# Optimization experiments

Hardware: AMD Instinct MI355X
Metric: run time of the kernel (lower is better)

Reference implementation:

```python
import jax, jax.numpy as jnp
import numpy as np

B, L_ENC, L_DEC, PRED_LEN = 16, 720, 144, 96
D_MODEL, N_HEADS, D_FF, M_FEAT = 512, 8, 2048, 256
ENC_IN, DEC_IN, C_OUT, MARK = 7, 7, 7, 4
E_LAYERS = 2
DH = D_MODEL // N_HEADS


def _orf(m, d, seed):
    # Gaussian orthogonal random features (FAVOR+), scaling=0 (chi-norm rows).
    rng = np.random.default_rng(seed)
    blocks = [np.linalg.qr(rng.standard_normal((d, d)))[0].T for _ in range(m // d)]
    mat = np.concatenate(blocks, 0)  # [m, d]
    mult = np.linalg.norm(rng.standard_normal((m, d)), axis=1)
    return jnp.asarray(mult[:, None] * mat, dtype=jnp.float32)

PROJ_ENC = [_orf(M_FEAT, DH, s) for s in range(E_LAYERS)]
PROJ_DEC_SELF = _orf(M_FEAT, DH, 10)
PROJ_DEC_CROSS = _orf(M_FEAT, DH, 11)


def _pos_emb(n, d):
    pos = np.arange(n, dtype=np.float32)[:, None]
    div = np.exp(np.arange(0, d, 2, dtype=np.float32) * (-np.log(10000.0) / d))
    pe = np.zeros((n, d), dtype=np.float32)
    pe[:, 0::2] = np.sin(pos * div)
    pe[:, 1::2] = np.cos(pos * div)
    return jnp.asarray(pe)

PE_ENC = _pos_emb(L_ENC, D_MODEL)
PE_DEC = _pos_emb(L_DEC, D_MODEL)


def layer_norm(x, g, b):
    mu = x.mean(-1, keepdims=True)
    var = ((x - mu) ** 2).mean(-1, keepdims=True)
    return (x - mu) / jnp.sqrt(var + 1e-5) * g + b


def feature_map(x, proj, is_query):
    # FAVOR+ positive softmax kernel. x: [b,h,n,dh], proj: [m,dh]
    norm = DH ** -0.25
    xd = jnp.einsum('bhnd,md->bhnm', x * norm, proj)
    diag = (x ** 2).sum(-1) * (0.5 * norm * norm)  # [b,h,n]
    if is_query:
        stab = jax.lax.stop_gradient(xd.max(axis=-1, keepdims=True))
    else:
        stab = jax.lax.stop_gradient(xd.max(axis=(-1, -2), keepdims=True))
    return (M_FEAT ** -0.5) * (jnp.exp(xd - diag[..., None] - stab) + 1e-4)


def noncausal_attn(q, k, v):
    kv = jnp.einsum('bhnm,bhnd->bhmd', k, v)
    d_inv = 1.0 / jnp.einsum('bhnm,bhm->bhn', q, k.sum(2))
    return jnp.einsum('bhnm,bhmd,bhn->bhnd', q, kv, d_inv)


def causal_attn(q, k, v):
    # prefix-sum linear attention; carry S [b,h,m,dh], s [b,h,m]
    b, h, n, m = q.shape
    dh = v.shape[-1]

    def step(carry, qkv):
        S, s = carry
        qn, kn, vn = qkv
        S = S + kn[..., None] * vn[..., None, :]
        s = s + kn
        num = jnp.einsum('bhm,bhmd->bhd', qn, S)
        den = jnp.einsum('bhm,bhm->bh', qn, s)
        return (S, s), num / (den[..., None] + 1e-6)

    init = (jnp.zeros((b, h, m, dh), q.dtype), jnp.zeros((b, h, m), q.dtype))
    _, out = jax.lax.scan(step, init, (jnp.moveaxis(q, 2, 0), jnp.moveaxis(k, 2, 0), jnp.moveaxis(v, 2, 0)))
    return jnp.moveaxis(out, 0, 2)


def attention(x, ctx, Wq, Wk, Wv, Wo, bo, proj, causal):
    b, n, _ = x.shape
    nc = ctx.shape[1]
    q = (x @ Wq).reshape(b, n, N_HEADS, DH).transpose(0, 2, 1, 3)
    k = (ctx @ Wk).reshape(b, nc, N_HEADS, DH).transpose(0, 2, 1, 3)
    v = (ctx @ Wv).reshape(b, nc, N_HEADS, DH).transpose(0, 2, 1, 3)
    qp = feature_map(q, proj, True)
    kp = feature_map(k, proj, False)
    o = causal_attn(qp, kp, v) if causal else noncausal_attn(qp, kp, v)
    o = o.transpose(0, 2, 1, 3).reshape(b, n, D_MODEL)
    return o @ Wo + bo


def embed(x, mark, conv_w, time_w, pe):
    # TokenEmbedding: circular conv1d k=3 (no bias) + fixed sinusoidal PE + timeF linear
    xp = jnp.concatenate([x[:, -1:], x, x[:, :1]], axis=1)
    tok = (jnp.einsum('blc,cd->bld', xp[:, :-2], conv_w[0])
           + jnp.einsum('blc,cd->bld', xp[:, 1:-1], conv_w[1])
           + jnp.einsum('blc,cd->bld', xp[:, 2:], conv_w[2]))
    return tok + pe[None] + mark @ time_w


def _forward(x_enc, x_mark_enc, x_dec, x_mark_dec,
             emb_conv_enc, emb_time_enc, emb_conv_dec, emb_time_dec,
             enc_Wq, enc_Wk, enc_Wv, enc_Wo, enc_bo,
             enc_ff1, enc_b1, enc_ff2, enc_b2, enc_ln_g, enc_ln_b, enc_fg, enc_fb,
             dec_sWq, dec_sWk, dec_sWv, dec_sWo, dec_sbo,
             dec_cWq, dec_cWk, dec_cWv, dec_cWo, dec_cbo,
             dec_ff1, dec_b1, dec_ff2, dec_b2, dec_ln_g, dec_ln_b, dec_fg, dec_fb,
             proj_w, proj_b):
    gelu = lambda t: jax.nn.gelu(t, approximate=False)
    # RevIN-style instance normalization (means detached, as in the torch code)
    means = jax.lax.stop_gradient(x_enc.mean(1, keepdims=True))
    xc = x_enc - means
    stdev = jnp.sqrt(xc.var(1, keepdims=True) + 1e-5)
    xe = xc / stdev

    enc = embed(xe, x_mark_enc, emb_conv_enc, emb_time_enc, PE_ENC)
    for i in range(E_LAYERS):
        a = attention(enc, enc, enc_Wq[i], enc_Wk[i], enc_Wv[i], enc_Wo[i], enc_bo[i], PROJ_ENC[i], False)
        x1 = layer_norm(enc + a, enc_ln_g[i, 0], enc_ln_b[i, 0])
        y = gelu(x1 @ enc_ff1[i] + enc_b1[i]) @ enc_ff2[i] + enc_b2[i]
        enc = layer_norm(x1 + y, enc_ln_g[i, 1], enc_ln_b[i, 1])
    enc = layer_norm(enc, enc_fg, enc_fb)

    dec = embed(x_dec, x_mark_dec, emb_conv_dec, emb_time_dec, PE_DEC)
    a = attention(dec, dec, dec_sWq, dec_sWk, dec_sWv, dec_sWo, dec_sbo, PROJ_DEC_SELF, True)
    x1 = layer_norm(dec + a, dec_ln_g[0], dec_ln_b[0])
    c = attention(x1, enc, dec_cWq, dec_cWk, dec_cWv, dec_cWo, dec_cbo, PROJ_DEC_CROSS, False)
    x2 = layer_norm(x1 + c, dec_ln_g[1], dec_ln_b[1])
    y = gelu(x2 @ dec_ff1 + dec_b1) @ dec_ff2 + dec_b2
    dec = layer_norm(x2 + y, dec_ln_g[2], dec_ln_b[2])
    dec = layer_norm(dec, dec_fg, dec_fb)
    out = dec @ proj_w + proj_b  # [B, L_DEC, C_OUT]

    out = out * stdev[:, 0][:, None, :] + means[:, 0][:, None, :]
    return out[:, -PRED_LEN:, :]


def setup_inputs():
    ks = iter(jax.random.split(jax.random.key(0), 48))

    def rn(shape, scale=1.0):
        return jax.random.normal(next(ks), shape, dtype=jnp.float32) * scale

    w = 0.02
    E, D, F = E_LAYERS, D_MODEL, D_FF
    return {
        'x_enc': rn((B, L_ENC, ENC_IN)),
        'x_mark_enc': rn((B, L_ENC, MARK)),
        'x_dec': rn((B, L_DEC, DEC_IN)),
        'x_mark_dec': rn((B, L_DEC, MARK)),
        'emb_conv_enc': rn((3, ENC_IN, D), 0.1),
        'emb_time_enc': rn((MARK, D), w),
        'emb_conv_dec': rn((3, DEC_IN, D), 0.1),
        'emb_time_dec': rn((MARK, D), w),
        'enc_Wq': rn((E, D, D), w), 'enc_Wk': rn((E, D, D), w),
        'enc_Wv': rn((E, D, D), w), 'enc_Wo': rn((E, D, D), w),
        'enc_bo': jnp.zeros((E, D), jnp.float32),
        'enc_ff1': rn((E, D, F), w), 'enc_b1': jnp.zeros((E, F), jnp.float32),
        'enc_ff2': rn((E, F, D), w), 'enc_b2': jnp.zeros((E, D), jnp.float32),
        'enc_ln_g': jnp.ones((E, 2, D), jnp.float32), 'enc_ln_b': jnp.zeros((E, 2, D), jnp.float32),
        'enc_fg': jnp.ones((D,), jnp.float32), 'enc_fb': jnp.zeros((D,), jnp.float32),
        'dec_sWq': rn((D, D), w), 'dec_sWk': rn((D, D), w), 'dec_sWv': rn((D, D), w), 'dec_sWo': rn((D, D), w),
        'dec_sbo': jnp.zeros((D,), jnp.float32),
        'dec_cWq': rn((D, D), w), 'dec_cWk': rn((D, D), w), 'dec_cWv': rn((D, D), w), 'dec_cWo': rn((D, D), w),
        'dec_cbo': jnp.zeros((D,), jnp.float32),
        'dec_ff1': rn((D, F), w), 'dec_b1': jnp.zeros((F,), jnp.float32),
        'dec_ff2': rn((F, D), w), 'dec_b2': jnp.zeros((D,), jnp.float32),
        'dec_ln_g': jnp.ones((3, D), jnp.float32), 'dec_ln_b': jnp.zeros((3, D), jnp.float32),
        'dec_fg': jnp.ones((D,), jnp.float32), 'dec_fb': jnp.zeros((D,), jnp.float32),
        'proj_w': rn((D, C_OUT), w), 'proj_b': jnp.zeros((C_OUT,), jnp.float32),
    }


def reference(x_enc, x_mark_enc, x_dec, x_mark_dec,
              emb_conv_enc, emb_time_enc, emb_conv_dec, emb_time_dec,
              enc_Wq, enc_Wk, enc_Wv, enc_Wo, enc_bo,
              enc_ff1, enc_b1, enc_ff2, enc_b2, enc_ln_g, enc_ln_b, enc_fg, enc_fb,
              dec_sWq, dec_sWk, dec_sWv, dec_sWo, dec_sbo,
              dec_cWq, dec_cWk, dec_cWv, dec_cWo, dec_cbo,
              dec_ff1, dec_b1, dec_ff2, dec_b2, dec_ln_g, dec_ln_b, dec_fg, dec_fb,
              proj_w, proj_b):
    return _forward(x_enc, x_mark_enc, x_dec, x_mark_dec,
                    emb_conv_enc, emb_time_enc, emb_conv_dec, emb_time_dec,
                    enc_Wq, enc_Wk, enc_Wv, enc_Wo, enc_bo,
                    enc_ff1, enc_b1, enc_ff2, enc_b2, enc_ln_g, enc_ln_b, enc_fg, enc_fb,
                    dec_sWq, dec_sWk, dec_sWv, dec_sWo, dec_sbo,
                    dec_cWq, dec_cWk, dec_cWv, dec_cWo, dec_cbo,
                    dec_ff1, dec_b1, dec_ff2, dec_b2, dec_ln_g, dec_ln_b, dec_fg, dec_fb,
                    proj_w, proj_b)
```

## Files before the change

### kernel.cpp

```cpp
#include <hip/hip_runtime.h>
#include <math.h>
#include <string.h>

#define BB    16
#define LEc   720
#define LDc   144
#define PREDc 96
#define DMc   512
#define NHc   8
#define DHc   64
#define MFc   256
#define FFc   2048
#define NEc   (BB*LEc)
#define NDc   (BB*LDc)
#define BHc   (BB*NHc)
#define KSn   ((size_t)BHc*MFc)

typedef unsigned int u32;
typedef unsigned short u16;
typedef unsigned long long u64;
typedef unsigned __int128 u128;

typedef short bfx8 __attribute__((ext_vector_type(8)));
typedef float fx4  __attribute__((ext_vector_type(4)));
// ... 105 lines not shown
    if (xnorm == 0.0){
      tau[j] = 0.0;
      for (int i=j;i<n;i++) V[j][i] = (i==j) ? 1.0 : 0.0;
      continue;
    }
    double beta = -copysign(hypot(alpha, xnorm), alpha);
    double tj = (beta - alpha)/beta;
    double sc = 1.0/(alpha - beta);
    tau[j] = tj;
    V[j][j] = 1.0;
    for (int i=j+1;i<n;i++) V[j][i] = A[i*n+j]*sc;
    A[j*n+j] = beta;
    for (int c=j+1;c<n;c++){
      double w = 0;
      for (int i=j;i<n;i++) w += V[j][i]*A[i*n+c];
      w *= tj;
      for (int i=j;i<n;i++) A[i*n+c] -= V[j][i]*w;
    }
  }
  for (int i=0;i<n;i++) for (int c=0;c<n;c++) Q[i*n+c] = (i==c)?1.0:0.0;
  for (int j=n-1;j>=0;j--){
    double tj = tau[j];
    if (tj == 0.0) continue;
    for (int c=0;c<n;c++){
      double w = 0;
      for (int i=j;i<n;i++) w += V[j][i]*Q[i*n+c];
      w *= tj;
      for (int i=j;i<n;i++) Q[i*n+c] -= V[j][i]*w;
    }
  }
}

static void build_orf(u32 seed, float* outp){
  NpPCG64 g(seed);
  static double mat[MFc][DHc];
  static double A[64*64], Q[64*64];
  for (int blk=0; blk<4; blk++){
    for (int i=0;i<4096;i++) A[i] = std_normal(g);
    qr_q64(A, Q);
    for (int r=0;r<64;r++)
      for (int c=0;c<64;c++)
        mat[blk*64 + r][c] = Q[c*64 + r];
  }
  for (int r=0;r<MFc;r++){
    double ss = 0;
    double row[64];
    for (int c=0;c<64;c++){ row[c] = std_normal(g); ss += row[c]*row[c]; }
    double nrm = sqrt(ss);
    for (int c=0;c<64;c++) outp[r*64 + c] = (float)(nrm * mat[r][c]);
  }
}

static void build_all_proj(float* h){
  init_zig();
  const u32 seeds[4] = {0u, 1u, 10u, 11u};
  for (int s=0;s<4;s++) build_orf(seeds[s], h + (size_t)s*MFc*DHc);
}

__device__ __forceinline__ u16 f2bf(float x){
  u32 u = __builtin_bit_cast(u32, x);
  u32 r = (u + 0x7FFFu + ((u >> 16) & 1u)) >> 16;
  return (u16)r;
}
__device__ __forceinline__ float bf2f(u16 x){
  return __builtin_bit_cast(float, ((u32)x) << 16);
}


__global__ __launch_bounds__(256) void k_zero(float* __restrict__ p, int n){
  int i = blockIdx.x*256 + threadIdx.x;
  if (i < n) p[i] = 0.f;
}

__global__ __launch_bounds__(256) void k_projbf(const float* __restrict__ p, u16* __restrict__ pb, int n){
  int i = blockIdx.x*256 + threadIdx.x;
  if (i < n) pb[i] = f2bf(p[i]);
}

__global__ __launch_bounds__(256) void k_petab(float* __restrict__ pe){
  int idx = blockIdx.x*256 + threadIdx.x;
  int d = idx & 511; int l = idx >> 9;
  int i2 = d & ~1;
  float div = expf((float)i2 * (-0.017988946039015984f));
  float ang = (float)l * div;
  pe[idx] = (d & 1) ? cosf(ang) : sinf(ang);
}

__global__ __launch_bounds__(256) void k_wtr(const float* __restrict__ W, u16* __restrict__ WT,
                                             int K, int N){
  __shared__ float t[32][33];
  int kb = blockIdx.x*32, nb = blockIdx.y*32;
  int tx = threadIdx.x & 31, ty = threadIdx.x >> 5;
  #pragma unroll
  for (int p=0;p<4;p++)
    t[ty + p*8][tx] = W[(size_t)(kb + ty + p*8)*N + nb + tx];
  __syncthreads();
  #pragma unroll
  for (int p=0;p<4;p++)
    WT[(size_t)(nb + ty + p*8)*K + kb + tx] = f2bf(t[tx][ty + p*8]);
}

__global__ __launch_bounds__(64) void k_meanstd(const float* __restrict__ x,
                                                float* __restrict__ means, float* __restrict__ stdev){
  int bc = blockIdx.x; int b = bc/7, c = bc%7;
  int t = threadIdx.x;
  float s=0;
  for (int l=t; l<LEc; l+=64) s += x[((size_t)b*LEc+l)*7 + c];
  for (int o=32;o;o>>=1) s += __shfl_down(s,o);
  s = __shfl(s,0);
  float mu = s / (float)LEc;
  float v=0;
  for (int l=t; l<LEc; l+=64){ float d = x[((size_t)b*LEc+l)*7+c]-mu; v += d*d; }
  for (int o=32;o;o>>=1) v += __shfl_down(v,o);
  if (t==0){ means[bc]=mu; stdev[bc]=sqrtf(v/(float)LEc + 1e-5f); }
}

__global__ __launch_bounds__(256) void k_embed(const float* __restrict__ x, const float* __restrict__ mark,
    const float* __restrict__ convw, const float* __restrict__ timew, const float* __restrict__ pe,
    const float* __restrict__ means, const float* __restrict__ stdev,
    int L, int donorm, float* __restrict__ outp)
{
  size_t idx = (size_t)blockIdx.x*256 + threadIdx.x;
  size_t total = (size_t)BB*L*DMc;
  if (idx >= total) return;
  int d = (int)(idx % DMc); size_t bl = idx / DMc; int l = (int)(bl % L); int b = (int)(bl / L);
  int lm = (l==0)? L-1 : l-1;
  int lp = (l==L-1)? 0 : l+1;
  float acc = pe[(size_t)l*DMc + d];
  const float* xb = x + (size_t)b*L*7;
  #pragma unroll
  for (int c=0;c<7;c++){
    float v0 = xb[(size_t)lm*7+c], v1 = xb[(size_t)l*7+c], v2 = xb[(size_t)lp*7+c];
    if (donorm){
      float mu = means[b*7+c], sd = stdev[b*7+c];
      v0=(v0-mu)/sd; v1=(v1-mu)/sd; v2=(v2-mu)/sd;
    }
    acc += v0*convw[(0*7+c)*DMc+d] + v1*convw[(1*7+c)*DMc+d] + v2*convw[(2*7+c)*DMc+d];
  }
  const float* mb = mark + ((size_t)b*L + l)*4;
  #pragma unroll
  for (int t=0;t<4;t++) acc += mb[t]*timew[t*DMc+d];
  outp[idx] = acc;
}

template<int A_BF16, int OUT_BF16, int GELU>
__global__ __launch_bounds__(256) void k_gemm_mfma(
    const void* __restrict__ Ap, const u16* __restrict__ WT,
    const float* __restrict__ bias, void* __restrict__ Cp,
    int M, int N, int K)
{
  __shared__ u16 As[128][40];
  __shared__ u16 Bs[128][40];
  int nb = N >> 7;
  int bx = blockIdx.x % nb, by = blockIdx.x / nb;
  int row0 = by << 7, col0 = bx << 7;
  int tid = threadIdx.x;
  int wid = tid >> 6, lane = tid & 63;
  int wr = (wid >> 1) * 64, wc = (wid & 1) * 64;
  int l15 = lane & 15, lg = lane >> 4;
  fx4 acc[4][4];
  #pragma unroll
  for (int i=0;i<4;i++)
    #pragma unroll
    for (int j=0;j<4;j++)
      #pragma unroll
      for (int r=0;r<4;r++) acc[i][j][r] = 0.f;

  for (int k0 = 0; k0 < K; k0 += 32){
    if (A_BF16){
      const u16* A = (const u16*)Ap;
      #pragma unroll
      for (int p=0;p<2;p++){
        int idx = tid + (p<<8);
        int r = idx >> 2, kq = (idx & 3) << 3;
        *(bfx8*)&As[r][kq] = *(const bfx8*)(A + (size_t)(row0+r)*K + k0 + kq);
      }
    } else {
      const float* A = (const float*)Ap;
      #pragma unroll
      for (int p=0;p<4;p++){
        int idx = tid + (p<<8);
        int r = idx >> 3, kq = (idx & 7) << 2;
        float4 v = *(const float4*)(A + (size_t)(row0+r)*K + k0 + kq);
        u32 lo = (u32)f2bf(v.x) | ((u32)f2bf(v.y) << 16);
        u32 hi = (u32)f2bf(v.z) | ((u32)f2bf(v.w) << 16);
        *(u32*)&As[r][kq]   = lo;
        *(u32*)&As[r][kq+2] = hi;
      }
    }
    #pragma unroll
    for (int p=0;p<2;p++){
      int idx = tid + (p<<8);
      int c = idx >> 2, kq = (idx & 3) << 3;
      *(bfx8*)&Bs[c][kq] = *(const bfx8*)(WT + (size_t)(col0+c)*K + k0 + kq);
    }
    __syncthreads();
    int kg = lg << 3;
    bfx8 af[4], bf[4];
    #pragma unroll
    for (int i=0;i<4;i++) af[i] = *(const bfx8*)&As[wr + i*16 + l15][kg];
    #pragma unroll
    for (int j=0;j<4;j++) bf[j] = *(const bfx8*)&Bs[wc + j*16 + l15][kg];
    #pragma unroll
    for (int i=0;i<4;i++)
      #pragma unroll
      for (int j=0;j<4;j++)
        acc[i][j] = __builtin_amdgcn_mfma_f32_16x16x32_bf16(af[i], bf[j], acc[i][j], 0, 0, 0);
    __syncthreads();
  }
  #pragma unroll
  for (int j=0;j<4;j++){
    int col = col0 + wc + j*16 + l15;
    float bv = bias ? bias[col] : 0.f;
    #pragma unroll
    for (int i=0;i<4;i++){
      #pragma unroll
      for (int r=0;r<4;r++){
        int row = row0 + wr + i*16 + (lg<<2) + r;
        float v = acc[i][j][r] + bv;
        if (GELU) v = 0.5f*v*(1.0f + erff(v*0.7071067811865475f));
        if (OUT_BF16) ((u16*)Cp)[(size_t)row*N + col] = f2bf(v);
        else          ((float*)Cp)[(size_t)row*N + col] = v;
      }
    }
  }
}

static inline void gemm_bf(const void* A, const u16* WT, const float* bias, void* C,
                           int M, int N, int K, int abf, int obf, int gelu, hipStream_t st){
  dim3 g((N/128)*(M/128));
  if (abf)            k_gemm_mfma<1,0,0><<<g,256,0,st>>>(A,WT,bias,C,M,N,K);
  else if (gelu)      k_gemm_mfma<0,1,1><<<g,256,0,st>>>(A,WT,bias,C,M,N,K);
  else if (obf)       k_gemm_mfma<0,1,0><<<g,256,0,st>>>(A,WT,bias,C,M,N,K);
  else                k_gemm_mfma<0,0,0><<<g,256,0,st>>>(A,WT,bias,C,M,N,K);
}

__global__ __launch_bounds__(256) void k_rowmax_mfma(const u16* __restrict__ Kb,
    const u16* __restrict__ projbf, float* __restrict__ rowmax, int n)
{
  int ntile = n >> 4;
  int rt = blockIdx.x % ntile, bh = blockIdx.x / ntile;
  int b = bh >> 3, h = bh & 7;
  int row0 = rt << 4;
  int tid = threadIdx.x, w = tid >> 6, lane = tid & 63;
  int l15 = lane & 15, lg = lane >> 4;
  __shared__ u16 qs[16][72];
  __shared__ float xds[16][264];
  __shared__ float red[16][16];
  for (int i = tid; i < 16*16; i += 256){
    int r = i >> 4, dq = (i & 15)*4;
    *(u16x4*)&qs[r][dq] = *(const u16x4*)(Kb + ((size_t)b*n + row0 + r)*DMc + h*64 + dq);
  }
  __syncthreads();
  #pragma unroll
  for (int mt=0; mt<4; mt++){
    int m16 = (w*4+mt)*16;
    fx4 a2 = {0.f,0.f,0.f,0.f};
    #pragma unroll
    for (int ks=0; ks<2; ks++){
      bfx8 af = *(const bfx8*)&qs[l15][ks*32 + lg*8];
      bfx8 bf = *(const bfx8*)(projbf + (size_t)(m16+l15)*64 + ks*32 + lg*8);
      a2 = __builtin_amdgcn_mfma_f32_16x16x32_bf16(af, bf, a2, 0, 0, 0);
    }
    #pragma unroll
    for (int r=0;r<4;r++)
      xds[lg*4+r][m16+l15] = a2[r];
  }
  __syncthreads();
  { int r = tid >> 4, s = tid & 15;
    float mx = -1e30f;
    #pragma unroll
    for (int j=0;j<16;j++) mx = fmaxf(mx, xds[r][s*16+j]);
    red[r][s] = mx; }
  __syncthreads();
  if (tid < 16){
    float mx = -1e30f;
    #pragma unroll
    for (int j=0;j<16;j++) mx = fmaxf(mx, red[tid][j]);
    rowmax[(size_t)bh*n + row0 + tid] = mx * 0.35355339059327373f;
  }
}

__global__ __launch_bounds__(256) void k_stab(const float* __restrict__ rowmax, float* __restrict__ stab, int n){
  int bh = blockIdx.x; int tid = threadIdx.x;
  float mx = -1e30f;
  for (int i=tid;i<n;i+=256) mx = fmaxf(mx, rowmax[(size_t)bh*n+i]);
  __shared__ float red[4];
  for (int o=32;o;o>>=1) mx = fmaxf(mx, __shfl_xor(mx,o));
  if ((tid&63)==0) red[tid>>6]=mx;
  __syncthreads();
  if (tid==0) stab[bh] = fmaxf(fmaxf(red[0],red[1]),fmaxf(red[2],red[3]));
}

__global__ __launch_bounds__(256) void k_vtr(const u16* __restrict__ Vb, u16* __restrict__ Vt, int n){
  int nt = n >> 4;
  int blk = blockIdx.x; int t16 = blk % nt; int bh = blk / nt;
  int b = bh >> 3, h = bh & 7;
  int n0 = t16 << 4;
  int t = threadIdx.x;
  __shared__ u16 vt[16][72];
  { int r = t >> 4, d0 = (t & 15) * 4;
    *(u16x4*)&vt[r][d0] = *(const u16x4*)(Vb + ((size_t)b*n + n0 + r)*DMc + h*64 + d0); }
  __syncthreads();
  { int d = t >> 2, j = t & 3;
    u16x4 o;
    o.x = vt[j*4+0][d]; o.y = vt[j*4+1][d]; o.z = vt[j*4+2][d]; o.w = vt[j*4+3][d];
    *(u16x4*)(Vt + ((size_t)bh*64 + d)*(size_t)n + n0 + j*4) = o; }
}

__global__ __launch_bounds__(256) void k_kvfull(const u16* __restrict__ Kb,
    const u16* __restrict__ Vt, const u16* __restrict__ projbf, const float* __restrict__ stab,
    u16* __restrict__ KVT, float* __restrict__ KS, int n)
{
  int bh = blockIdx.x >> 1; int dh = (blockIdx.x & 1) * 32;
  int b = bh >> 3, h = bh & 7;
  int tid = threadIdx.x, w = tid >> 6, lane = tid & 63;
  int l15 = lane & 15, lg = lane >> 4;
  float sb = stab[bh];
  __shared__ u16 ksb[32][72];
  __shared__ u16 kpT[256][40];
  __shared__ u16 vsb[32][40];
  __shared__ float dgs[32];
  fx4 kv[2][4];
  #pragma unroll
  for (int i=0;i<2;i++)
    #pragma unroll
    for (int j=0;j<4;j++)
      #pragma unroll
      for (int r=0;r<4;r++) kv[i][j][r] = 0.f;
  float ksl[4] = {0.f,0.f,0.f,0.f};
  int nchunks = (n + 31) >> 5;
  for (int c=0; c<nchunks; c++){
    int n0 = c << 5;
    for (int i = tid; i < 32*16; i += 256){
      int r = i >> 4, dq = (i & 15) * 4;
      u16x4 v = {0,0,0,0};
      if (n0 + r < n) v = *(const u16x4*)(Kb + ((size_t)b*n + n0 + r)*DMc + h*64 + dq);
      *(u16x4*)&ksb[r][dq] = v;
    }
    for (int i = tid; i < 32*8; i += 256){
      int r = i >> 3, nq4 = (i & 7) * 4;
      u16x4 v = {0,0,0,0};
      const u16* src = Vt + ((size_t)bh*64 + dh + r)*(size_t)n + n0 + nq4;
      if (n0 + nq4 + 3 < n) v = *(const u16x4*)src;
      else { for (int j=0;j<4;j++) if (n0+nq4+j < n) v[j] = src[j]; }
      *(u16x4*)&vsb[r][nq4] = v;
    }
    __syncthreads();
    {
      int r = tid >> 3, j = tid & 7;
      float dg = 0;
      #pragma unroll
      for (int q=0;q<8;q++){ float kd = bf2f(ksb[r][j*8+q]); dg = fmaf(kd,kd,dg); }
      dg += __shfl_down(dg,4); dg += __shfl_down(dg,2); dg += __shfl_down(dg,1);
      if (j == 0) dgs[r] = dg * 0.0625f;
    }
    __syncthreads();
    #pragma unroll
    for (int mt=0; mt<4; mt++){
      int m16 = (w*4 + mt)*16;
      #pragma unroll
      for (int nt=0; nt<2; nt++){
        fx4 a2 = {0.f,0.f,0.f,0.f};
        #pragma unroll
        for (int ks=0; ks<2; ks++){
          bfx8 af = *(const bfx8*)&ksb[nt*16 + l15][ks*32 + lg*8];
          bfx8 bf = *(const bfx8*)(projbf + (size_t)(m16 + l15)*64 + ks*32 + lg*8);
          a2 = __builtin_amdgcn_mfma_f32_16x16x32_bf16(af, bf, a2, 0, 0, 0);
        }
        #pragma unroll
        for (int r=0;r<4;r++){
          int nn = nt*16 + lg*4 + r;
          float kp = 0.f;
          if (n0 + nn < n)
            kp = (expf(a2[r]*0.35355339059327373f - dgs[nn] - sb) + 1e-4f) * 0.0625f;
          ksl[mt] += kp;
          kpT[m16 + l15][nn] = f2bf(kp);
        }
      }
    }
    __syncthreads();
    #pragma unroll
    for (int dt=0; dt<2; dt++){
      #pragma unroll
      for (int mt=0; mt<4; mt++){
        bfx8 af = *(const bfx8*)&vsb[dt*16 + l15][lg*8];
        bfx8 bf = *(const bfx8*)&kpT[(w*4+mt)*16 + l15][lg*8];
        kv[dt][mt] = __builtin_amdgcn_mfma_f32_16x16x32_bf16(af, bf, kv[dt][mt], 0, 0, 0);
      }
    }
    __syncthreads();
  }
  if (dh == 0){
    #pragma unroll
    for (int mt=0; mt<4; mt++){
      float v = ksl[mt];
      v += __shfl_xor(v, 16);
      v += __shfl_xor(v, 32);
      if (lg == 0) KS[(size_t)bh*MFc + (w*4+mt)*16 + l15] = v;
    }
  }
  #pragma unroll
  for (int dt=0; dt<2; dt++)
    #pragma unroll
    for (int mt=0; mt<4; mt++)
      #pragma unroll
      for (int r=0;r<4;r++){
        int d = dh + dt*16 + lg*4 + r;
        int m = (w*4+mt)*16 + l15;
        KVT[((size_t)bh*64 + d)*MFc + m] = f2bf(kv[dt][mt][r]);
      }
}

__global__ __launch_bounds__(256) void k_attn_mfma(const u16* __restrict__ Qb,
    const u16* __restrict__ projbf, const u16* __restrict__ KVT, const float* __restrict__ KS,
    u16* __restrict__ O, int nq)
{
  int ntile = nq >> 4;
  int rt = blockIdx.x % ntile, bh = blockIdx.x / ntile;
  int b = bh >> 3, h = bh & 7;
  int row0 = rt << 4;
  int tid = threadIdx.x, w = tid >> 6, lane = tid & 63;
  int l15 = lane & 15, lg = lane >> 4;
  __shared__ u16 qs[16][72];
  __shared__ float xds[16][264];
  __shared__ u16 qpl[16][264];
  __shared__ float dgs[16], mxs[16], dns[16];
  __shared__ float red[16][16];
  __shared__ float kss[256];
  for (int i = tid; i < 16*16; i += 256){
    int r = i >> 4, dq = (i & 15)*4;
    *(u16x4*)&qs[r][dq] = *(const u16x4*)(Qb + ((size_t)b*nq + row0 + r)*DMc + h*64 + dq);
  }
  kss[tid] = KS[(size_t)bh*MFc + tid];
  __syncthreads();
  if (tid < 16){
    float dg = 0;
    #pragma unroll 16
    for (int d=0;d<64;d++){ float q = bf2f(qs[tid][d]); dg = fmaf(q,q,dg); }
    dgs[tid] = dg * 0.0625f;
  }
  #pragma unroll
  for (int mt=0; mt<4; mt++){
    int m16 = (w*4+mt)*16;
    fx4 a2 = {0.f,0.f,0.f,0.f};
    #pragma unroll
    for (int ks=0; ks<2; ks++){
      bfx8 af = *(const bfx8*)&qs[l15][ks*32 + lg*8];
      bfx8 bf = *(const bfx8*)(projbf + (size_t)(m16+l15)*64 + ks*32 + lg*8);
      a2 = __builtin_amdgcn_mfma_f32_16x16x32_bf16(af, bf, a2, 0, 0, 0);
    }
    #pragma unroll
    for (int r=0;r<4;r++)
      xds[lg*4+r][m16+l15] = a2[r]*0.35355339059327373f;
  }
  __syncthreads();
  { int r = tid >> 4, s = tid & 15;
    float mx = -1e30f;
    #pragma unroll
    for (int j=0;j<16;j++) mx = fmaxf(mx, xds[r][s*16+j]);
    red[r][s] = mx; }
  __syncthreads();
  if (tid < 16){
    float mx = -1e30f;
    #pragma unroll
    for (int j=0;j<16;j++) mx = fmaxf(mx, red[tid][j]);
    mxs[tid] = mx;
  }
  __syncthreads();
  { int r = tid >> 4, s = tid & 15;
    float dg = dgs[r], mx = mxs[r], pd = 0;
    #pragma unroll
    for (int j=0;j<16;j++){
      int m = s*16+j;
      float v = (expf(xds[r][m] - dg - mx) + 1e-4f)*0.0625f;
      qpl[r][m] = f2bf(v);
      pd = fmaf(v, kss[m], pd);
    }
    red[r][s] = pd; }
  __syncthreads();
  if (tid < 16){
    float s = 0;
    #pragma unroll
    for (int j=0;j<16;j++) s += red[tid][j];
    dns[tid] = 1.0f / s;
  }
  __syncthreads();
  fx4 a2 = {0.f,0.f,0.f,0.f};
  #pragma unroll
  for (int ks=0; ks<8; ks++){
    bfx8 af = *(const bfx8*)&qpl[l15][ks*32 + lg*8];
    bfx8 bf = *(const bfx8*)(KVT + ((size_t)bh*64 + w*16 + l15)*MFc + ks*32 + lg*8);
    a2 = __builtin_amdgcn_mfma_f32_16x16x32_bf16(af, bf, a2, 0, 0, 0);
  }
  #pragma unroll
  for (int r=0;r<4;r++){
    int row = lg*4 + r;
    O[((size_t)b*nq + row0 + row)*DMc + h*64 + w*16 + l15] = f2bf(a2[r]*dns[row]);
  }
}

template<int ISQ>
__global__ __launch_bounds__(256) void k_fmap_mfma(const u16* __restrict__ Xb,
    const u16* __restrict__ projbf, const float* __restrict__ stab,
    u16* __restrict__ P, int n)
{
  int ntile = n >> 4;
  int rt = blockIdx.x % ntile, bh = blockIdx.x / ntile;
  int b = bh >> 3, h = bh & 7;
  int row0 = rt << 4;
  int tid = threadIdx.x, w = tid >> 6, lane = tid & 63;
  int l15 = lane & 15, lg = lane >> 4;
  __shared__ u16 qs[16][72];
  __shared__ float xds[16][264];
  __shared__ float dgs[16], mxs[16];
  __shared__ float red[16][16];
  for (int i = tid; i < 16*16; i += 256){
    int r = i >> 4, dq = (i & 15)*4;
    *(u16x4*)&qs[r][dq] = *(const u16x4*)(Xb + ((size_t)b*n + row0 + r)*DMc + h*64 + dq);
  }
  __syncthreads();
  if (tid < 16){
    float dg = 0;
    #pragma unroll 16
    for (int d=0;d<64;d++){ float q = bf2f(qs[tid][d]); dg = fmaf(q,q,dg); }
    dgs[tid] = dg * 0.0625f;
  }
  #pragma unroll
  for (int mt=0; mt<4; mt++){
    int m16 = (w*4+mt)*16;
    fx4 a2 = {0.f,0.f,0.f,0.f};
    #pragma unroll
    for (int ks=0; ks<2; ks++){
      bfx8 af = *(const bfx8*)&qs[l15][ks*32 + lg*8];
      bfx8 bf = *(const bfx8*)(projbf + (size_t)(m16+l15)*64 + ks*32 + lg*8);
      a2 = __builtin_amdgcn_mfma_f32_16x16x32_bf16(af, bf, a2, 0, 0, 0);
    }
    #pragma unroll
    for (int r=0;r<4;r++)
      xds[lg*4+r][m16+l15] = a2[r]*0.35355339059327373f;
  }
  __syncthreads();
  if (ISQ){
    { int r = tid >> 4, s = tid & 15;
      float mx = -1e30f;
      #pragma unroll
      for (int j=0;j<16;j++) mx = fmaxf(mx, xds[r][s*16+j]);
      red[r][s] = mx; }
    __syncthreads();
    if (tid < 16){
      float mx = -1e30f;
      #pragma unroll
      for (int j=0;j<16;j++) mx = fmaxf(mx, red[tid][j]);
      mxs[tid] = mx;
    }
    __syncthreads();
  }
  { int r = tid >> 4, s = tid & 15;
    float sv = ISQ ? mxs[r] : stab[bh];
    float dg = dgs[r];
    u16* dst = P + ((size_t)bh*n + row0 + r)*MFc;
    #pragma unroll
    for (int j=0;j<16;j++){
      int m = s*16+j;
      dst[m] = f2bf((expf(xds[r][m] - dg - sv) + 1e-4f)*0.0625f);
    }
  }
}

__global__ __launch_bounds__(256) void k_causal_mfma(const u16* __restrict__ PQ,
    const u16* __restrict__ PK, const u16* __restrict__ Vt, u16* __restrict__ O, int n)
{
  int ntile = n >> 4;
  int it = blockIdx.x % ntile, bh = blockIdx.x / ntile;
  int b = bh >> 3, h = bh & 7;
  int row0 = it << 4;
  int tid = threadIdx.x, w = tid >> 6, lane = tid & 63;
  int l15 = lane & 15, lg = lane >> 4;
  __shared__ u16 qp[16][264];
  __shared__ float sf[16][168];
  __shared__ u16 sb[16][168];
  __shared__ u16 vt[64][168];
  __shared__ float dns[16];
  __shared__ float red[16][16];
  #pragma unroll
  for (int p=0;p<4;p++){
    int idx = tid + (p<<8);
    int r = idx >> 6, c4 = (idx & 63)*4;
    *(u16x4*)&qp[r][c4] = *(const u16x4*)(PQ + ((size_t)bh*n + row0 + r)*MFc + c4);
  }
  for (int i = tid; i < 64*40; i += 256){
    int r = i / 40, c4 = (i % 40)*4;
    u16x4 v = {0,0,0,0};
    if (c4 < 144) v = *(const u16x4*)(Vt + ((size_t)bh*64 + r)*(size_t)n + c4);
    *(u16x4*)&vt[r][c4] = v;
  }
  { int r = tid >> 4, c = 144 + (tid & 15);
    sb[r][c] = 0; sf[r][c] = 0.f; }
  __syncthreads();
  for (int jt = w; jt < 9; jt += 4){
    fx4 a2 = {0.f,0.f,0.f,0.f};
    #pragma unroll
    for (int ks=0; ks<8; ks++){
      bfx8 af = *(const bfx8*)&qp[l15][ks*32 + lg*8];
      bfx8 bf = *(const bfx8*)(PK + ((size_t)bh*n + jt*16 + l15)*MFc + ks*32 + lg*8);
      a2 = __builtin_amdgcn_mfma_f32_16x16x32_bf16(af, bf, a2, 0, 0, 0);
    }
    int jg = jt*16 + l15;
    #pragma unroll
    for (int r=0;r<4;r++){
      int il = lg*4 + r;
      float v = (jg <= row0 + il) ? a2[r] : 0.f;
      sf[il][jg] = v;
      sb[il][jg] = f2bf(v);
    }
  }
  __syncthreads();
  { int r = tid >> 4, s = tid & 15;
    float pd = 0;
    #pragma unroll
    for (int q=0;q<9;q++) pd += sf[r][s*9 + q];
    red[r][s] = pd; }
  __syncthreads();
  if (tid < 16){
    float s = 0;
    #pragma unroll
    for (int j=0;j<16;j++) s += red[tid][j];
    dns[tid] = 1.0f / (s + 1e-6f);
  }
  __syncthreads();
  fx4 a2 = {0.f,0.f,0.f,0.f};
  #pragma unroll
  for (int ks=0; ks<5; ks++){
    bfx8 af = *(const bfx8*)&sb[l15][ks*32 + lg*8];
    bfx8 bf = *(const bfx8*)&vt[w*16 + l15][ks*32 + lg*8];
    a2 = __builtin_amdgcn_mfma_f32_16x16x32_bf16(af, bf, a2, 0, 0, 0);
  }
  #pragma unroll
  for (int r=0;r<4;r++){
    int il = lg*4 + r;
    O[((size_t)b*n + row0 + il)*DMc + h*64 + w*16 + l15] = f2bf(a2[r]*dns[il]);
  }
}

__global__ __launch_bounds__(128) void k_ln(const float* __restrict__ A, const float* __restrict__ Bres,
    const float* __restrict__ g, const float* __restrict__ beta, float* __restrict__ outp)
{
  size_t row = blockIdx.x; int t = threadIdx.x;
  float4 v = *(const float4*)(A + row*DMc + t*4);
  if (Bres){ float4 w = *(const float4*)(Bres + row*DMc + t*4); v.x+=w.x; v.y+=w.y; v.z+=w.z; v.w+=w.w; }
  __shared__ float red[2];
  float s = v.x+v.y+v.z+v.w;
  for (int o=32;o;o>>=1) s += __shfl_xor(s,o);
  if ((t&63)==0) red[t>>6]=s;
  __syncthreads();
  float mu = (red[0]+red[1]) * (1.0f/DMc);
  float dx=v.x-mu, dy=v.y-mu, dz=v.z-mu, dw=v.w-mu;
  float qq = dx*dx+dy*dy+dz*dz+dw*dw;
  __syncthreads();
  for (int o=32;o;o>>=1) qq += __shfl_xor(qq,o);
  if ((t&63)==0) red[t>>6]=qq;
  __syncthreads();
  float var = (red[0]+red[1]) * (1.0f/DMc);
  float rs = 1.0f / sqrtf(var + 1e-5f);
  const float4 g4 = *(const float4*)(g + t*4);
  const float4 b4 = *(const float4*)(beta + t*4);
  float4 o4;
  o4.x = dx*rs*g4.x + b4.x;
  o4.y = dy*rs*g4.y + b4.y;
  o4.z = dz*rs*g4.z + b4.z;
  o4.w = dw*rs*g4.w + b4.w;
  *(float4*)(outp + row*DMc + t*4) = o4;
}

__global__ __launch_bounds__(64) void k_final(const float* __restrict__ X, const float* __restrict__ pw,
   const float* __restrict__ pb, const float* __restrict__ means, const float* __restrict__ stdev,
   float* __restrict__ outp)
{
  int blk = blockIdx.x; int lo = blk % PREDc; int b = blk / PREDc;
  int l = lo + (LDc - PREDc);
  int t = threadIdx.x;
  float acc[7];
  #pragma unroll
  for (int c=0;c<7;c++) acc[c]=0;
  const float* xr = X + ((size_t)b*LDc + l)*DMc;
  for (int d=t; d<DMc; d+=64){
    float xv = xr[d];
    #pragma unroll
    for (int c=0;c<7;c++) acc[c] = fmaf(xv, pw[d*7+c], acc[c]);
  }
  #pragma unroll
  for (int c=0;c<7;c++){
    float s = acc[c];
    for (int o=32;o;o>>=1) s += __shfl_xor(s,o);
    if (t==0)
      outp[((size_t)b*PREDc + lo)*7 + c] = (s + pb[c]) * stdev[b*7+c] + means[b*7+c];
  }
}

extern "C" void kernel_launch(void* const* d_in, const int* in_sizes, int n_in,
                              void* d_out, int out_size, void* d_ws, size_t ws_size,
                              hipStream_t stream)
{
  (void)in_sizes; (void)n_in;
  const float* x_enc        = (const float*)d_in[0];
  const float* x_mark_enc   = (const float*)d_in[1];
  const float* x_dec        = (const float*)d_in[2];
  const float* x_mark_dec   = (const float*)d_in[3];
  const float* emb_conv_enc = (const float*)d_in[4];
  const float* emb_time_enc = (const float*)d_in[5];
  const float* emb_conv_dec = (const float*)d_in[6];
  const float* emb_time_dec = (const float*)d_in[7];
  const float* enc_Wq = (const float*)d_in[8];
  const float* enc_Wk = (const float*)d_in[9];
  const float* enc_Wv = (const float*)d_in[10];
  const float* enc_Wo = (const float*)d_in[11];
  const float* enc_bo = (const float*)d_in[12];
  const float* enc_ff1 = (const float*)d_in[13];
  const float* enc_b1  = (const float*)d_in[14];
  const float* enc_ff2 = (const float*)d_in[15];
  const float* enc_b2  = (const float*)d_in[16];
  const float* enc_ln_g = (const float*)d_in[17];
  const float* enc_ln_b = (const float*)d_in[18];
  const float* enc_fg = (const float*)d_in[19];
  const float* enc_fb = (const float*)d_in[20];
  const float* dec_sWq = (const float*)d_in[21];
  const float* dec_sWk = (const float*)d_in[22];
  const float* dec_sWv = (const float*)d_in[23];
  const float* dec_sWo = (const float*)d_in[24];
  const float* dec_sbo = (const float*)d_in[25];
  const float* dec_cWq = (const float*)d_in[26];
  const float* dec_cWk = (const float*)d_in[27];
  const float* dec_cWv = (const float*)d_in[28];
  const float* dec_cWo = (const float*)d_in[29];
  const float* dec_cbo = (const float*)d_in[30];
  const float* dec_ff1 = (const float*)d_in[31];
  const float* dec_b1  = (const float*)d_in[32];
  const float* dec_ff2 = (const float*)d_in[33];
  const float* dec_b2  = (const float*)d_in[34];
  const float* dec_ln_g = (const float*)d_in[35];
  const float* dec_ln_b = (const float*)d_in[36];
  const float* dec_fg = (const float*)d_in[37];
  const float* dec_fb = (const float*)d_in[38];
  const float* proj_w = (const float*)d_in[39];
  const float* proj_b = (const float*)d_in[40];
  float* outp = (float*)d_out;
  float* W = (float*)d_ws;

  size_t o = 0;
  #define ALLOCF(nm, n) size_t nm = o; o += (((size_t)(n)) + 63) & ~(size_t)63;
  ALLOCF(o_proj, 4*MFc*DHc)
  ALLOCF(o_projbf, 2*MFc*DHc)
  ALLOCF(o_means, BB*7)
  ALLOCF(o_std,   BB*7)
  ALLOCF(o_rmE, (size_t)BHc*LEc)
  ALLOCF(o_rmD, (size_t)BHc*LDc)
  ALLOCF(o_stab, BHc)
  ALLOCF(o_KS, KSn)
  ALLOCF(o_PE, (size_t)LEc*DMc)
  ALLOCF(o_Dx1, (size_t)NDc*DMc)
  ALLOCF(o_WT, 5242880)
  ALLOCF(o_Xb, (size_t)NEc*DMc)
  ALLOCF(o_X1, (size_t)NEc*DMc)
  ALLOCF(o_U,  11796480)
  #undef ALLOCF
  size_t needed_bytes = o * sizeof(float);
  if (ws_size < needed_bytes){
    k_zero<<<(out_size+255)/256, 256, 0, stream>>>(outp, out_size);
    return;
  }

  float* Xb  = W + o_Xb;
  float* X1  = W + o_X1;
  float* KS  = W + o_KS;
  float* PE  = W + o_PE;
  float* rmE = W + o_rmE;
  float* rmD = W + o_rmD;
  float* stb = W + o_stab;
  u16*  WTb = (u16*)(W + o_WT);
  u16*  Uh  = (u16*)(W + o_U);
  u16*  PJB = (u16*)(W + o_projbf);

  const size_t NEu = (size_t)NEc*DMc;
  const size_t NDu = (size_t)NDc*DMc;
  u16* Tq = Uh;            u16* Tk = Uh + NEu;
  u16* Tv = Uh + 2*NEu;    u16* Oe = Uh + 3*NEu;
  u16* FFb = Uh;
  u16*   VtU  = (u16*)X1;
  u16*   KVTu = (u16*)(X1 + 2949120);
  u16* dTq = Uh;           u16* dTk = Uh + NDu;
  u16* dTv = Uh + 2*NDu;   u16* dOd = Uh + 3*NDu;
  u16* PQb = Uh + 4*NDu;
  u16* PKb = PQb + (size_t)BHc*LDc*MFc;
  u16* VtD = PKb + (size_t)BHc*LDc*MFc;
  u16* cTk = Uh;           u16* cTv = Uh + NEu;
  u16* dTq2 = Uh + 2*NEu;  u16* cOd = Uh + 2*NEu + NDu;
  u16* dFF = Uh;
  float* DX  = X1 + 0*NDu;
  float* Da  = X1 + 1*NDu;
  float* Dx2 = X1 + 2*NDu;
  float* Dy  = X1 + 3*NDu;
  float* Dx1 = W + o_Dx1;

  static float h_proj[4*MFc*DHc];
  build_all_proj(h_proj);
  hipMemcpyAsync(W + o_proj, h_proj, sizeof(h_proj), hipMemcpyHostToDevice, stream);
  k_projbf<<<(4*MFc*DHc)/256, 256, 0, stream>>>(W + o_proj, PJB, 4*MFc*DHc);
  const u16* pb_enc0  = PJB + 0*MFc*DHc;
  const u16* pb_enc1  = PJB + 1*MFc*DHc;
  const u16* pb_self  = PJB + 2*MFc*DHc;
  const u16* pb_cross = PJB + 3*MFc*DHc;

  k_petab<<<(LEc*DMc)/256, 256, 0, stream>>>(PE);

  size_t wto = 0;
  auto xpose = [&](const float* Wsrc, int K, int N) -> const u16* {
    u16* dst = WTb + wto; wto += (size_t)K*N;
    k_wtr<<<dim3(K/32, N/32), 256, 0, stream>>>(Wsrc, dst, K, N);
    return dst;
  };
  const u16 *wQ[2], *wK[2], *wV[2], *wO[2], *wF1[2], *wF2[2];
  for (int i=0;i<2;i++){
    wQ[i]  = xpose(enc_Wq + (size_t)i*DMc*DMc, DMc, DMc);
    wK[i]  = xpose(enc_Wk + (size_t)i*DMc*DMc, DMc, DMc);
    wV[i]  = xpose(enc_Wv + (size_t)i*DMc*DMc, DMc, DMc);
    wO[i]  = xpose(enc_Wo + (size_t)i*DMc*DMc, DMc, DMc);
    wF1[i] = xpose(enc_ff1 + (size_t)i*DMc*FFc, DMc, FFc);
    wF2[i] = xpose(enc_ff2 + (size_t)i*FFc*DMc, FFc, DMc);
  }
  const u16* wsQ = xpose(dec_sWq, DMc, DMc);
  const u16* wsK = xpose(dec_sWk, DMc, DMc);
  const u16* wsV = xpose(dec_sWv, DMc, DMc);
  const u16* wsO = xpose(dec_sWo, DMc, DMc);
  const u16* wcQ = xpose(dec_cWq, DMc, DMc);
  const u16* wcK = xpose(dec_cWk, DMc, DMc);
  const u16* wcV = xpose(dec_cWv, DMc, DMc);
  const u16* wcO = xpose(dec_cWo, DMc, DMc);
  const u16* wdF1 = xpose(dec_ff1, DMc, FFc);
  const u16* wdF2 = xpose(dec_ff2, FFc, DMc);

  auto kv_chain = [&](const u16* Kbuf, const u16* Vbuf, const u16* pjb){
    k_rowmax_mfma<<<BHc*(LEc/16), 256, 0, stream>>>(Kbuf, pjb, rmE, LEc);
    k_stab<<<BHc, 256, 0, stream>>>(rmE, stb, LEc);
    k_vtr<<<BHc*(LEc/16), 256, 0, stream>>>(Vbuf, VtU, LEc);
    k_kvfull<<<BHc*2, 256, 0, stream>>>(Kbuf, VtU, pjb, stb, KVTu, KS, LEc);
  };

  k_meanstd<<<BB*7, 64, 0, stream>>>(x_enc, W+o_means, W+o_std);
  k_embed<<<(BB*LEc*DMc)/256, 256, 0, stream>>>(x_enc, x_mark_enc, emb_conv_enc, emb_time_enc,
                                                PE, W+o_means, W+o_std, LEc, 1, Xb);

  for (int i=0;i<2;i++){
    const float* bo = enc_bo + (size_t)i*DMc;
    const float* b1 = enc_b1  + (size_t)i*FFc;
    const float* b2 = enc_b2  + (size_t)i*DMc;
    const float* g0 = enc_ln_g + (size_t)(i*2+0)*DMc;
    const float* e0 = enc_ln_b + (size_t)(i*2+0)*DMc;
    const float* g1 = enc_ln_g + (size_t)(i*2+1)*DMc;
    const float* e1 = enc_ln_b + (size_t)(i*2+1)*DMc;
    const u16*   pjb = (i==0) ? pb_enc0 : pb_enc1;

    gemm_bf(Xb, wQ[i], nullptr, Tq, NEc, DMc, DMc, 0,1,0, stream);
    gemm_bf(Xb, wK[i], nullptr, Tk, NEc, DMc, DMc, 0,1,0, stream);
    gemm_bf(Xb, wV[i], nullptr, Tv, NEc, DMc, DMc, 0,1,0, stream);
    kv_chain(Tk, Tv, pjb);
    k_attn_mfma<<<BHc*(LEc/16), 256, 0, stream>>>(Tq, pjb, KVTu, KS, Oe, LEc);
    gemm_bf(Oe, wO[i], bo, X1, NEc, DMc, DMc, 1,0,0, stream);
    k_ln<<<NEc, 128, 0, stream>>>(X1, Xb, g0, e0, X1);
    gemm_bf(X1, wF1[i], b1, FFb, NEc, FFc, DMc, 0,1,1, stream);
    gemm_bf(FFb, wF2[i], b2, Xb, NEc, DMc, FFc, 1,0,0, stream);
    k_ln<<<NEc, 128, 0, stream>>>(Xb, X1, g1, e1, Xb);
  }
  k_ln<<<NEc, 128, 0, stream>>>(Xb, nullptr, enc_fg, enc_fb, Xb);

  k_embed<<<(BB*LDc*DMc)/256, 256, 0, stream>>>(x_dec, x_mark_dec, emb_conv_dec, emb_time_dec,
                                                PE, W+o_means, W+o_std, LDc, 0, DX);
  gemm_bf(DX, wsQ, nullptr, dTq, NDc, DMc, DMc, 0,1,0, stream);
  gemm_bf(DX, wsK, nullptr, dTk, NDc, DMc, DMc, 0,1,0, stream);
  gemm_bf(DX, wsV, nullptr, dTv, NDc, DMc, DMc, 0,1,0, stream);
  k_rowmax_mfma<<<BHc*(LDc/16), 256, 0, stream>>>(dTk, pb_self, rmD, LDc);
  k_stab<<<BHc, 256, 0, stream>>>(rmD, stb, LDc);
  k_fmap_mfma<1><<<BHc*(LDc/16), 256, 0, stream>>>(dTq, pb_self, nullptr, PQb, LDc);
  k_fmap_mfma<0><<<BHc*(LDc/16), 256, 0, stream>>>(dTk, pb_self, stb, PKb, LDc);
  k_vtr<<<BHc*(LDc/16), 256, 0, stream>>>(dTv, VtD, LDc);
  k_causal_mfma<<<BHc*(LDc/16), 256, 0, stream>>>(PQb, PKb, VtD, dOd, LDc);
  gemm_bf(dOd, wsO, dec_sbo, Da, NDc, DMc, DMc, 1,0,0, stream);
  k_ln<<<NDc, 128, 0, stream>>>(Da, DX, dec_ln_g + 0*DMc, dec_ln_b + 0*DMc, Dx1);

  gemm_bf(Dx1, wcQ, nullptr, dTq2, NDc, DMc, DMc, 0,1,0, stream);
  gemm_bf(Xb,  wcK, nullptr, cTk,  NEc, DMc, DMc, 0,1,0, stream);
  gemm_bf(Xb,  wcV, nullptr, cTv,  NEc, DMc, DMc, 0,1,0, stream);
  kv_chain(cTk, cTv, pb_cross);
  k_attn_mfma<<<BHc*(LDc/16), 256, 0, stream>>>(dTq2, pb_cross, KVTu, KS, cOd, LDc);
  gemm_bf(cOd, wcO, dec_cbo, Da, NDc, DMc, DMc, 1,0,0, stream);
  k_ln<<<NDc, 128, 0, stream>>>(Da, Dx1, dec_ln_g + 1*DMc, dec_ln_b + 1*DMc, Dx2);

  gemm_bf(Dx2, wdF1, dec_b1, dFF, NDc, FFc, DMc, 0,1,1, stream);
  gemm_bf(dFF, wdF2, dec_b2, Dy, NDc, DMc, FFc, 1,0,0, stream);
  k_ln<<<NDc, 128, 0, stream>>>(Dy, Dx2, dec_ln_g + 2*DMc, dec_ln_b + 2*DMc, Da);
  k_ln<<<NDc, 128, 0, stream>>>(Da, nullptr, dec_fg, dec_fb, Da);
  k_final<<<BB*PREDc, 64, 0, stream>>>(Da, proj_w, proj_b, W+o_means, W+o_std, outp);
}
```

Baseline: 1.494 ms.

## Store intermediate activations in bf16, remap GEMM blocks, use fast exp

```diff
diff --git a/kernel.cpp b/kernel.cpp
--- a/kernel.cpp
+++ b/kernel.cpp
@@ -281,7 +281,10 @@
   __shared__ u16 As[128][40];
   __shared__ u16 Bs[128][40];
   int nb = N >> 7;
-  int bx = blockIdx.x % nb, by = blockIdx.x / nb;
+  int bid = blockIdx.x;
+  int nwg = gridDim.x;
+  if (!(nwg & 7)) bid = ((bid & 7) * (nwg >> 3)) + (bid >> 3);
+  int bx = bid % nb, by = bid / nb;
   int row0 = by << 7, col0 = bx << 7;
   int tid = threadIdx.x;
   int wid = tid >> 6, lane = tid & 63;
@@ -358,10 +361,12 @@
 static inline void gemm_bf(const void* A, const u16* WT, const float* bias, void* C,
                            int M, int N, int K, int abf, int obf, int gelu, hipStream_t st){
   dim3 g((N/128)*(M/128));
-  if (abf)            k_gemm_mfma<1,0,0><<<g,256,0,st>>>(A,WT,bias,C,M,N,K);
-  else if (gelu)      k_gemm_mfma<0,1,1><<<g,256,0,st>>>(A,WT,bias,C,M,N,K);
-  else if (obf)       k_gemm_mfma<0,1,0><<<g,256,0,st>>>(A,WT,bias,C,M,N,K);
-  else                k_gemm_mfma<0,0,0><<<g,256,0,st>>>(A,WT,bias,C,M,N,K);
+  if (abf && obf && gelu)  k_gemm_mfma<1,1,1><<<g,256,0,st>>>(A,WT,bias,C,M,N,K);
+  else if (abf && obf)     k_gemm_mfma<1,1,0><<<g,256,0,st>>>(A,WT,bias,C,M,N,K);
+  else if (abf)            k_gemm_mfma<1,0,0><<<g,256,0,st>>>(A,WT,bias,C,M,N,K);
+  else if (gelu)           k_gemm_mfma<0,1,1><<<g,256,0,st>>>(A,WT,bias,C,M,N,K);
+  else if (obf)            k_gemm_mfma<0,1,0><<<g,256,0,st>>>(A,WT,bias,C,M,N,K);
+  else                     k_gemm_mfma<0,0,0><<<g,256,0,st>>>(A,WT,bias,C,M,N,K);
 }
 
 __global__ __launch_bounds__(256) void k_rowmax_mfma(const u16* __restrict__ Kb,
@@ -502,7 +507,7 @@
           int nn = nt*16 + lg*4 + r;
           float kp = 0.f;
           if (n0 + nn < n)
-            kp = (expf(a2[r]*0.35355339059327373f - dgs[nn] - sb) + 1e-4f) * 0.0625f;
+            kp = (__expf(a2[r]*0.35355339059327373f - dgs[nn] - sb) + 1e-4f) * 0.0625f;
           ksl[mt] += kp;
           kpT[m16 + l15][nn] = f2bf(kp);
         }
@@ -602,7 +607,7 @@
     #pragma unroll
     for (int j=0;j<16;j++){
       int m = s*16+j;
-      float v = (expf(xds[r][m] - dg - mx) + 1e-4f)*0.0625f;
+      float v = (__expf(xds[r][m] - dg - mx) + 1e-4f)*0.0625f;
       qpl[r][m] = f2bf(v);
       pd = fmaf(v, kss[m], pd);
     }
@@ -692,7 +697,7 @@
     #pragma unroll
     for (int j=0;j<16;j++){
       int m = s*16+j;
-      dst[m] = f2bf((expf(xds[r][m] - dg - sv) + 1e-4f)*0.0625f);
+      dst[m] = f2bf((__expf(xds[r][m] - dg - sv) + 1e-4f)*0.0625f);
     }
   }
 }
@@ -772,12 +777,27 @@
   }
 }
 
-__global__ __launch_bounds__(128) void k_ln(const float* __restrict__ A, const float* __restrict__ Bres,
-    const float* __restrict__ g, const float* __restrict__ beta, float* __restrict__ outp)
+template<int ABF, int RBF, int OBF>
+__global__ __launch_bounds__(128) void k_ln(const void* __restrict__ Ap, const void* __restrict__ Rp,
+    const float* __restrict__ g, const float* __restrict__ beta, void* __restrict__ outp)
 {
   size_t row = blockIdx.x; int t = threadIdx.x;
-  float4 v = *(const float4*)(A + row*DMc + t*4);
-  if (Bres){ float4 w = *(const float4*)(Bres + row*DMc + t*4); v.x+=w.x; v.y+=w.y; v.z+=w.z; v.w+=w.w; }
+  float4 v;
+  if (ABF){
+    u16x4 a = *((const u16x4*)Ap + row*(DMc/4) + t);
+    v.x = bf2f(a.x); v.y = bf2f(a.y); v.z = bf2f(a.z); v.w = bf2f(a.w);
+  } else {
+    v = *((const float4*)Ap + row*(DMc/4) + t);
+  }
+  if (Rp){
+    if (RBF){
+      u16x4 wv = *((const u16x4*)Rp + row*(DMc/4) + t);
+      v.x += bf2f(wv.x); v.y += bf2f(wv.y); v.z += bf2f(wv.z); v.w += bf2f(wv.w);
+    } else {
+      float4 wv = *((const float4*)Rp + row*(DMc/4) + t);
+      v.x += wv.x; v.y += wv.y; v.z += wv.z; v.w += wv.w;
+    }
+  }
   __shared__ float red[2];
   float s = v.x+v.y+v.z+v.w;
   for (int o=32;o;o>>=1) s += __shfl_xor(s,o);
@@ -794,12 +814,17 @@
   float rs = 1.0f / sqrtf(var + 1e-5f);
   const float4 g4 = *(const float4*)(g + t*4);
   const float4 b4 = *(const float4*)(beta + t*4);
-  float4 o4;
-  o4.x = dx*rs*g4.x + b4.x;
-  o4.y = dy*rs*g4.y + b4.y;
-  o4.z = dz*rs*g4.z + b4.z;
-  o4.w = dw*rs*g4.w + b4.w;
-  *(float4*)(outp + row*DMc + t*4) = o4;
+  float ox = dx*rs*g4.x + b4.x;
+  float oy = dy*rs*g4.y + b4.y;
+  float oz = dz*rs*g4.z + b4.z;
+  float ow = dw*rs*g4.w + b4.w;
+  if (OBF){
+    u16x4 o4; o4.x=f2bf(ox); o4.y=f2bf(oy); o4.z=f2bf(oz); o4.w=f2bf(ow);
+    *((u16x4*)outp + row*(DMc/4) + t) = o4;
+  } else {
+    float4 o4; o4.x=ox; o4.y=oy; o4.z=oz; o4.w=ow;
+    *((float4*)outp + row*(DMc/4) + t) = o4;
+  }
 }
 
 __global__ __launch_bounds__(64) void k_final(const float* __restrict__ X, const float* __restrict__ pw,
@@ -917,6 +942,8 @@
   u16* FFb = Uh;
   u16*   VtU  = (u16*)X1;
   u16*   KVTu = (u16*)(X1 + 2949120);
+  u16*   x1bf   = (u16*)X1;
+  u16*   attnbf = (u16*)X1 + NEu;
   u16* dTq = Uh;           u16* dTk = Uh + NDu;
   u16* dTv = Uh + 2*NDu;   u16* dOd = Uh + 3*NDu;
   u16* PQb = Uh + 4*NDu;
@@ -929,7 +956,9 @@
   float* Da  = X1 + 1*NDu;
   float* Dx2 = X1 + 2*NDu;
   float* Dy  = X1 + 3*NDu;
-  float* Dx1 = W + o_Dx1;
+  u16* dAttnbf = (u16*)Da;
+  u16* Dx1bf   = (u16*)(W + o_Dx1);
+  u16* Dx2bf   = (u16*)Dx2;
 
   static float h_proj[4*MFc*DHc];
   build_all_proj(h_proj);
@@ -994,13 +1023,13 @@
     gemm_bf(Xb, wV[i], nullptr, Tv, NEc, DMc, DMc, 0,1,0, stream);
     kv_chain(Tk, Tv, pjb);
     k_attn_mfma<<<BHc*(LEc/16), 256, 0, stream>>>(Tq, pjb, KVTu, KS, Oe, LEc);
-    gemm_bf(Oe, wO[i], bo, X1, NEc, DMc, DMc, 1,0,0, stream);
-    k_ln<<<NEc, 128, 0, stream>>>(X1, Xb, g0, e0, X1);
-    gemm_bf(X1, wF1[i], b1, FFb, NEc, FFc, DMc, 0,1,1, stream);
+    gemm_bf(Oe, wO[i], bo, attnbf, NEc, DMc, DMc, 1,1,0, stream);
+    k_ln<1,0,1><<<NEc, 128, 0, stream>>>(attnbf, Xb, g0, e0, x1bf);
+    gemm_bf(x1bf, wF1[i], b1, FFb, NEc, FFc, DMc, 1,1,1, stream);
     gemm_bf(FFb, wF2[i], b2, Xb, NEc, DMc, FFc, 1,0,0, stream);
-    k_ln<<<NEc, 128, 0, stream>>>(Xb, X1, g1, e1, Xb);
-  }
-  k_ln<<<NEc, 128, 0, stream>>>(Xb, nullptr, enc_fg, enc_fb, Xb);
+    k_ln<0,1,0><<<NEc, 128, 0, stream>>>(Xb, x1bf, g1, e1, Xb);
+  }
+  k_ln<0,0,0><<<NEc, 128, 0, stream>>>(Xb, nullptr, enc_fg, enc_fb, Xb);
 
   k_embed<<<(BB*LDc*DMc)/256, 256, 0, stream>>>(x_dec, x_mark_dec, emb_conv_dec, emb_time_dec,
                                                 PE, W+o_means, W+o_std, LDc, 0, DX);
@@ -1013,20 +1042,20 @@
   k_fmap_mfma<0><<<BHc*(LDc/16), 256, 0, stream>>>(dTk, pb_self, stb, PKb, LDc);
   k_vtr<<<BHc*(LDc/16), 256, 0, stream>>>(dTv, VtD, LDc);
   k_causal_mfma<<<BHc*(LDc/16), 256, 0, stream>>>(PQb, PKb, VtD, dOd, LDc);
-  gemm_bf(dOd, wsO, dec_sbo, Da, NDc, DMc, DMc, 1,0,0, stream);
-  k_ln<<<NDc, 128, 0, stream>>>(Da, DX, dec_ln_g + 0*DMc, dec_ln_b + 0*DMc, Dx1);
-
-  gemm_bf(Dx1, wcQ, nullptr, dTq2, NDc, DMc, DMc, 0,1,0, stream);
+  gemm_bf(dOd, wsO, dec_sbo, dAttnbf, NDc, DMc, DMc, 1,1,0, stream);
+  k_ln<1,0,1><<<NDc, 128, 0, stream>>>(dAttnbf, DX, dec_ln_g + 0*DMc, dec_ln_b + 0*DMc, Dx1bf);
+
+  gemm_bf(Dx1bf, wcQ, nullptr, dTq2, NDc, DMc, DMc, 1,1,0, stream);
   gemm_bf(Xb,  wcK, nullptr, cTk,  NEc, DMc, DMc, 0,1,0, stream);
   gemm_bf(Xb,  wcV, nullptr, cTv,  NEc, DMc, DMc, 0,1,0, stream);
   kv_chain(cTk, cTv, pb_cross);
   k_attn_mfma<<<BHc*(LDc/16), 256, 0, stream>>>(dTq2, pb_cross, KVTu, KS, cOd, LDc);
   gemm_bf(cOd, wcO, dec_cbo, Da, NDc, DMc, DMc, 1,0,0, stream);
-  k_ln<<<NDc, 128, 0, stream>>>(Da, Dx1, dec_ln_g + 1*DMc, dec_ln_b + 1*DMc, Dx2);
-
-  gemm_bf(Dx2, wdF1, dec_b1, dFF, NDc, FFc, DMc, 0,1,1, stream);
+  k_ln<0,1,1><<<NDc, 128, 0, stream>>>(Da, Dx1bf, dec_ln_g + 1*DMc, dec_ln_b + 1*DMc, Dx2bf);
+
+  gemm_bf(Dx2bf, wdF1, dec_b1, dFF, NDc, FFc, DMc, 1,1,1, stream);
   gemm_bf(dFF, wdF2, dec_b2, Dy, NDc, DMc, FFc, 1,0,0, stream);
-  k_ln<<<NDc, 128, 0, stream>>>(Dy, Dx2, dec_ln_g + 2*DMc, dec_ln_b + 2*DMc, Da);
-  k_ln<<<NDc, 128, 0, stream>>>(Da, nullptr, dec_fg, dec_fb, Da);
+  k_ln<0,1,0><<<NDc, 128, 0, stream>>>(Dy, Dx2bf, dec_ln_g + 2*DMc, dec_ln_b + 2*DMc, Da);
+  k_ln<0,0,0><<<NDc, 128, 0, stream>>>(Da, nullptr, dec_fg, dec_fb, Da);
   k_final<<<BB*PREDc, 64, 0, stream>>>(Da, proj_w, proj_b, W+o_means, W+o_std, outp);
 }
```

Measured after the change: 1.343 ms, median of 3. 1.11x faster.
